# Kernel tuning notes

Measured on AMD Instinct MI355X. Metric: run time of the kernel, lower is better.

The kernel has to match this reference:

```python
import jax, jax.numpy as jnp
import numpy as np

N = 20000      # nodes in both graphs
B = 128        # graphs in batch
E = 320000     # edges (avg degree 16)
F_IN = 768     # num_features (bert/graph feature dim)
RAW_F = 5000   # raw feature dim (hardcoded 5000 in source)
H = 256        # nhid
C = 4          # num_classes


def _gcn(x, src, dst, W, b):
    # PyG GCNConv: add self loops, symmetric D^-1/2 (A+I) D^-1/2 normalization
    n = x.shape[0]
    h = x @ W
    loop = jnp.arange(n, dtype=src.dtype)
    s = jnp.concatenate([src, loop])
    d = jnp.concatenate([dst, loop])
    deg = jax.ops.segment_sum(jnp.ones_like(d, dtype=h.dtype), d, num_segments=n)
    dinv = jax.lax.rsqrt(jnp.maximum(deg, 1.0))
    norm = (dinv[s] * dinv[d])[:, None]
    out = jax.ops.segment_sum(h[s] * norm, d, num_segments=n)
    return out + b


def _segment_mean(x, seg, num_segments):
    s = jax.ops.segment_sum(x, seg, num_segments=num_segments)
    cnt = jax.ops.segment_sum(jnp.ones((x.shape[0],), x.dtype), seg, num_segments=num_segments)
    return s / jnp.maximum(cnt, 1.0)[:, None]


def _prelu(x, a):
    return jnp.where(x >= 0, x, a * x)


def setup_inputs():
    key = jax.random.key(0)
    k = jax.random.split(key, 16)
    graph_x = jax.random.normal(k[0], (N, F_IN), jnp.float32)
    bert_x = jax.random.normal(k[1], (N, F_IN), jnp.float32)
    data_x = jax.random.normal(k[2], (N, RAW_F), jnp.float32) * 0.05
    edge_index = jax.random.randint(k[3], (2, E), 0, N, jnp.int32)
    raw_edge_index = jax.random.randint(k[4], (2, E), 0, N, jnp.int32)
    batch = ((jnp.arange(N) * B) // N).astype(jnp.int32)  # sorted, covers all B graphs
    rootindex = jax.random.randint(k[5], (B,), 0, N, jnp.int32)

    def lin(kk, fin, fout):
        return jax.random.normal(kk, (fin, fout), jnp.float32) * (1.0 / np.sqrt(fin))

    W1 = lin(k[6], F_IN, H); b1 = jnp.zeros((H,), jnp.float32)
    Wc0 = lin(k[7], RAW_F, H); bc0 = jnp.zeros((H,), jnp.float32)
    Wc1 = lin(k[8], H, H); bc1 = jnp.zeros((H,), jnp.float32)
    Wc2 = lin(k[9], H, H); bc2 = jnp.zeros((H,), jnp.float32)
    Wl1 = lin(k[10], 2 * RAW_F, 2 * H); bl1 = jnp.zeros((2 * H,), jnp.float32)
    Wl2 = lin(k[11], 2 * H, H); bl2 = jnp.zeros((H,), jnp.float32)
    W5 = lin(k[12], 5 * H, C); b5 = jnp.zeros((C,), jnp.float32)
    prelu_a = jnp.asarray(0.25, jnp.float32)
    return dict(graph_x=graph_x, bert_x=bert_x, data_x=data_x,
                edge_index=edge_index, raw_edge_index=raw_edge_index,
                graph_batch=batch, x_batch=batch, rootindex=rootindex,
                W1=W1, b1=b1, Wc0=Wc0, bc0=bc0, Wc1=Wc1, bc1=bc1, Wc2=Wc2, bc2=bc2,
                Wl1=Wl1, bl1=bl1, Wl2=Wl2, bl2=bl2, prelu_a=prelu_a, W5=W5, b5=b5)


def reference(graph_x, bert_x, data_x, edge_index, raw_edge_index, graph_batch,
              x_batch, rootindex, W1, b1, Wc0, bc0, Wc1, bc1, Wc2, bc2,
              Wl1, bl1, Wl2, bl2, prelu_a, W5, b5):
    # branch 1: GCNConv over graph_x (bert_user=0), relu, global max pool
    x = jax.nn.relu(_gcn(graph_x, edge_index[0], edge_index[1], W1, b1))
    x = jax.ops.segment_max(x, graph_batch, num_segments=B)   # [B, H]
    # branch 2: scatter_mean of raw features + root node, MLP w/ PReLU (eval: dropout = id)
    new_x = _segment_mean(data_x, x_batch, B)                 # [B, RAW_F]
    root = data_x[rootindex]                                  # [B, RAW_F]
    new_x = jnp.concatenate([new_x, root], axis=1)            # [B, 2*RAW_F]
    new_x = _prelu(new_x @ Wl1 + bl1, prelu_a)
    new_x = _prelu(new_x @ Wl2 + bl2, prelu_a)                # [B, H]
    # branch 3 (boost=1): 3 GCN layers over raw graph, mean pool each layer
    x_one = data_x
    pools = []
    for (W, b) in ((Wc0, bc0), (Wc1, bc1), (Wc2, bc2)):
        x_one = jax.nn.relu(_gcn(x_one, raw_edge_index[0], raw_edge_index[1], W, b))
        pools.append(_segment_mean(x_one, x_batch, B))
    out = jnp.concatenate(pools + [new_x, x], axis=1)         # [B, 5*H]
    return jax.nn.log_softmax(out @ W5 + b5, axis=1)
```

## Files before the change

### kernel.cpp

```cpp
#include <hip/hip_runtime.h>
#include <math.h>

#define NN   20000
#define BG   128
#define EE   320000
#define FIN  768
#define RAWF 5000
#define KP   5120
#define CATK 10240
#define HD   256
#define NC   4

typedef __attribute__((ext_vector_type(4))) float          f32x4;
typedef __attribute__((ext_vector_type(8))) unsigned short u16x8;
typedef __attribute__((ext_vector_type(4))) unsigned short u16x4;
typedef __attribute__((ext_vector_type(8))) __bf16         bf16x8;

__device__ __forceinline__ unsigned short f2bf(float f) {
  unsigned u = __float_as_uint(f);
  u += 0x7FFFu + ((u >> 16) & 1u);
  return (unsigned short)(u >> 16);
}
__device__ __forceinline__ float bf2f(unsigned short u) {
  return __uint_as_float((unsigned)u << 16);
}

static inline int ceil_div(int a, int b) { return (a + b - 1) / b; }

__global__ void count_deg2_k(const int* __restrict__ ei, const int* __restrict__ rei,
                             int* __restrict__ deg1, int* __restrict__ deg2) {
  int i = blockIdx.x * 256 + threadIdx.x;
  if (i < EE) atomicAdd(&deg1[ei[EE + i]], 1);
  else if (i < 2 * EE) atomicAdd(&deg2[rei[i]], 1);
}

__global__ __launch_bounds__(1024) void scan_local_k(const int* __restrict__ deg1,
                                                     const int* __restrict__ deg2,
                                                     int* __restrict__ excl,
                                                     int* __restrict__ bsum, int nb) {
  const int* deg = blockIdx.y ? deg2 : deg1;
  int* ex = excl + (size_t)blockIdx.y * NN;
  int* bs = bsum + (size_t)blockIdx.y * nb;
  __shared__ int wsum[16];
  int t = threadIdx.x, lane = t & 63, w = t >> 6;
  int i = blockIdx.x * 1024 + t;
  int v = (i < NN) ? deg[i] : 0;
  int acc = v;
#pragma unroll
  for (int off = 1; off < 64; off <<= 1) {
    int o = __shfl_up(acc, off, 64);
    if (lane >= off) acc += o;
  }
  if (lane == 63) wsum[w] = acc;
  __syncthreads();
  if (w == 0 && lane < 16) {
    int s = wsum[lane];
#pragma unroll
    for (int off = 1; off < 16; off <<= 1) {
      int o = __shfl_up(s, off, 64);
      if (lane >= off) s += o;
    }
    wsum[lane] = s;
  }
  __syncthreads();
  if (w > 0) acc += wsum[w - 1];
  if (i < NN) ex[i] = acc - v;
  if (t == 1023) bs[blockIdx.x] = acc;
}

__global__ void scan_tops_k(const int* __restrict__ bsum, int* __restrict__ boff,
                            int* __restrict__ end1, int* __restrict__ end2, int nb) {
  int t = threadIdx.x;
  int half = t >> 5, idx = t & 31;
  int v = (idx < nb) ? bsum[half * nb + idx] : 0;
  int acc = v;
#pragma unroll
  for (int off = 1; off < 32; off <<= 1) {
    int o = __shfl_up(acc, off, 32);
    if (idx >= off) acc += o;
  }
  if (idx < nb) boff[half * nb + idx] = acc - v;
  if (idx == nb - 1) {
    if (half == 0) *end1 = acc; else *end2 = acc;
  }
}

__global__ __launch_bounds__(1024) void scan_add_k(
    const int* __restrict__ excl, const int* __restrict__ boff,
    const int* __restrict__ deg1, const int* __restrict__ deg2,
    int* __restrict__ rp1, int* __restrict__ rp2,
    int* __restrict__ cur1, int* __restrict__ cur2,
    float* __restrict__ dv1, float* __restrict__ dv2,
    const int* __restrict__ batch, int* __restrict__ segs, int* __restrict__ sege,
    int nb) {
  int y = blockIdx.y;
  const int* deg = y ? deg2 : deg1;
  int* rp = y ? rp2 : rp1;
  int* cur = y ? cur2 : cur1;
  float* dv = y ? dv2 : dv1;
  int i = blockIdx.x * 1024 + threadIdx.x;
  if (i < NN) {
    int v = excl[(size_t)y * NN + i] + boff[y * nb + blockIdx.x];
    rp[i] = v;
    cur[i] = v;
    dv[i] = rsqrtf((float)(deg[i] + 1));
    if (y == 0) {
      int b = batch[i];
      if (i == 0 || batch[i - 1] != b) segs[b] = i;
      if (i == NN - 1 || batch[i + 1] != b) sege[b] = i + 1;
    }
  }
}

__global__ void scatter_k(const int* __restrict__ ei, const int* __restrict__ rei,
                          int* __restrict__ cur1, int* __restrict__ cur2,
                          int* __restrict__ col1, int* __restrict__ col2) {
  int i = blockIdx.x * 256 + threadIdx.x;
  int y = blockIdx.y;
  if (i < EE) {
    const int* e = y ? rei : ei;
    int* cur = y ? cur2 : cur1;
    int* col = y ? col2 : col1;
    int d = e[EE + i];
    int p = atomicAdd(&cur[d], 1);
    col[p] = e[i];
  }
}

__global__ __launch_bounds__(256) void trans_k(
    const float* __restrict__ i0, unsigned short* __restrict__ o0,
    const float* __restrict__ i1, unsigned short* __restrict__ o1,
    const float* __restrict__ i2, unsigned short* __restrict__ o2,
    const float* __restrict__ i3, unsigned short* __restrict__ o3,
    const float* __restrict__ i4, unsigned short* __restrict__ o4) {
  __shared__ unsigned short tile[32][34];
  int b = blockIdx.x;
  const float* in; unsigned short* out;
  int K, N, Kout, tx, lid;
  if (b < 192)        { in=i0; out=o0; K=768;   N=256; Kout=768;   tx=24;  lid=b; }
  else if (b < 1472)  { in=i1; out=o1; K=5000;  N=256; Kout=5120;  tx=160; lid=b-192; }
  else if (b < 1536)  { in=i2; out=o2; K=256;   N=256; Kout=256;   tx=8;   lid=b-1472; }
  else if (b < 1600)  { in=i3; out=o3; K=256;   N=256; Kout=256;   tx=8;   lid=b-1536; }
  else                { in=i4; out=o4; K=10000; N=512; Kout=10240; tx=320; lid=b-1600; }
  int k0 = (lid % tx) * 32, n0 = (lid / tx) * 32;
  int txx = threadIdx.x & 31, tyy = threadIdx.x >> 5;
#pragma unroll
  for (int r = 0; r < 32; r += 8) {
    int k = k0 + tyy + r, n = n0 + txx;
    float v = (k < K) ? in[(size_t)k * N + n] : 0.f;
    tile[tyy + r][txx] = f2bf(v);
  }
  __syncthreads();
#pragma unroll
  for (int r = 0; r < 32; r += 8) {
    int n = n0 + tyy + r, k = k0 + txx;
    out[(size_t)n * Kout + k] = tile[txx][tyy + r];
  }
}

__global__ __launch_bounds__(256) void conv_pool_k(const float* __restrict__ x,
                                                   unsigned short* __restrict__ xb,
                                                   unsigned short* __restrict__ cat,
                                                   const int* __restrict__ segs,
                                                   const int* __restrict__ sege,
                                                   const int* __restrict__ root) {
  int g = blockIdx.x;
  if (blockIdx.y >= KP / 256) {
    int c = (blockIdx.y - KP / 256) * 256 + threadIdx.x;
    if (c < CATK - RAWF) {
      unsigned short v = 0;
      if (c < RAWF) v = f2bf(x[(size_t)root[g] * RAWF + c]);
      cat[(size_t)g * CATK + RAWF + c] = v;
    }
    return;
  }
  __shared__ f32x4 part[4][64];
  int wave = threadIdx.x >> 6, lane = threadIdx.x & 63;
  int c = blockIdx.y * 256 + lane * 4;
  int s = segs[g], e = sege[g];
  bool v4 = (c + 4 <= RAWF);
  f32x4 sum = (f32x4)0.f;
  for (int i = s + wave; i < e; i += 4) {
    f32x4 v = (f32x4)0.f;
    if (v4) v = *(const f32x4*)(x + (size_t)i * RAWF + c);
    if (xb) {
      u16x4 h;
      h[0] = f2bf(v[0]); h[1] = f2bf(v[1]); h[2] = f2bf(v[2]); h[3] = f2bf(v[3]);
      *(u16x4*)(xb + (size_t)i * KP + c) = h;
    }
    sum += v;
  }
  part[wave][lane] = sum;
  __syncthreads();
  if (threadIdx.x < 64 && v4) {
    f32x4 tot = part[0][lane] + part[1][lane] + part[2][lane] + part[3][lane];
    float cnt = (float)(e - s);
    u16x4 o;
    o[0] = f2bf(tot[0] / cnt); o[1] = f2bf(tot[1] / cnt);
    o[2] = f2bf(tot[2] / cnt); o[3] = f2bf(tot[3] / cnt);
    *(u16x4*)(cat + (size_t)g * CATK + c) = o;
  }
}

template <bool ABF16>
__global__ __launch_bounds__(256) void gemm_k(
    const void* __restrict__ Av, int Astride,
    const unsigned short* __restrict__ Bt, int Bstride,
    float* __restrict__ C, unsigned short* __restrict__ Cb,
    const float* __restrict__ escale,
    int M, int N, int Kreal, int kchunk, int atomic_out) {
  __shared__ unsigned short As[128 * 40];
  __shared__ unsigned short Bs[128 * 40];
  const int tid = threadIdx.x;
  const int lane = tid & 63, wave = tid >> 6;
  const int quad = lane >> 4, l16 = lane & 15;
  const int koff = quad * 8;

  int xt = blockIdx.x, yt = blockIdx.y;
  if (gridDim.x == 2) {
    const int MT = gridDim.y;
    int flat = (yt << 1) | xt;
    int gp = flat >> 4;
    int ybase = gp << 3;
    int rem = MT - ybase;
    int j = flat & 15;
    if (rem >= 8) { xt = j >> 3; yt = ybase + (j & 7); }
    else          { xt = (j >= rem); yt = ybase + (xt ? j - rem : j); }
  }
  const int bn = xt * 128, bm = yt * 128;
  const int wm = (wave >> 1) * 64, wn = (wave & 1) * 64;
  const int kbegin = blockIdx.z * kchunk;
  int kend = kbegin + kchunk; if (kend > Kreal) kend = Kreal;

  const int brow = tid >> 2, bcol = (tid & 3) * 8;
  const int arow_f = tid >> 3, acol_f = (tid & 7) * 4;

  u16x8 pb[2];
  u16x8 pa_b[2];
  f32x4 pa_f[4];

  auto load_tile = [&](int k0) {
#pragma unroll
    for (int i = 0; i < 2; ++i) {
      int gk = k0 + bcol;
      bool ok = ABF16 ? true : (gk + 8 <= kend);
      u16x8 v = (u16x8)(unsigned short)0;
      if (ok) v = *(const u16x8*)(Bt + (size_t)(bn + i * 64 + brow) * Bstride + gk);
      pb[i] = v;
    }
    if (ABF16) {
      const unsigned short* A = (const unsigned short*)Av;
#pragma unroll
      for (int i = 0; i < 2; ++i) {
        int r = bm + i * 64 + brow;
        u16x8 v = (u16x8)(unsigned short)0;
        if (r < M) v = *(const u16x8*)(A + (size_t)r * Astride + k0 + bcol);
        pa_b[i] = v;
      }
    } else {
      const float* A = (const float*)Av;
#pragma unroll
      for (int i = 0; i < 4; ++i) {
        int r = bm + i * 32 + arow_f;
        int gk = k0 + acol_f;
        f32x4 v = (f32x4)0.f;
        if (r < M && gk + 4 <= kend) v = *(const f32x4*)(A + (size_t)r * Astride + gk);
        pa_f[i] = v;
      }
    }
  };
  auto store_tile = [&]() {
#pragma unroll
    for (int i = 0; i < 2; ++i)
      *(u16x8*)&Bs[(i * 64 + brow) * 40 + bcol] = pb[i];
    if (ABF16) {
#pragma unroll
      for (int i = 0; i < 2; ++i)
        *(u16x8*)&As[(i * 64 + brow) * 40 + bcol] = pa_b[i];
    } else {
#pragma unroll
      for (int i = 0; i < 4; ++i) {
        u16x4 h;
        h[0] = f2bf(pa_f[i][0]); h[1] = f2bf(pa_f[i][1]);
        h[2] = f2bf(pa_f[i][2]); h[3] = f2bf(pa_f[i][3]);
        *(u16x4*)&As[(i * 32 + arow_f) * 40 + acol_f] = h;
      }
    }
  };

  f32x4 acc[4][4] = {};
  load_tile(kbegin);
  for (int k0 = kbegin; k0 < kend; k0 += 32) {
    store_tile();
    __syncthreads();
    int k1 = k0 + 32;
    if (k1 < kend) load_tile(k1);
    u16x8 ar[4], br[4];
#pragma unroll
    for (int i = 0; i < 4; ++i) ar[i] = *(const u16x8*)&As[(wm + i * 16 + l16) * 40 + koff];
#pragma unroll
    for (int j = 0; j < 4; ++j) br[j] = *(const u16x8*)&Bs[(wn + j * 16 + l16) * 40 + koff];
#pragma unroll
    for (int i = 0; i < 4; ++i)
#pragma unroll
      for (int j = 0; j < 4; ++j)
        acc[i][j] = __builtin_amdgcn_mfma_f32_16x16x32_bf16(
            __builtin_bit_cast(bf16x8, ar[i]), __builtin_bit_cast(bf16x8, br[j]),
            acc[i][j], 0, 0, 0);
    __syncthreads();
  }
#pragma unroll
  for (int i = 0; i < 4; ++i)
#pragma unroll
    for (int rr = 0; rr < 4; ++rr) {
      int grow = bm + wm + i * 16 + quad * 4 + rr;
      if (grow >= M) continue;
      float sc = escale ? escale[grow] : 1.f;
#pragma unroll
      for (int j = 0; j < 4; ++j) {
        int gcol = bn + wn + j * 16 + l16;
        if (gcol >= N) continue;
        float v = acc[i][j][rr] * sc;
        if (Cb) Cb[(size_t)grow * N + gcol] = f2bf(v);
        else if (atomic_out) atomicAdd(&C[(size_t)grow * N + gcol], v);
        else C[(size_t)grow * N + gcol] = v;
      }
    }
}

__global__ void conv_h_k(const float* __restrict__ in, unsigned short* __restrict__ out) {
  size_t i = (size_t)(blockIdx.x * 256 + threadIdx.x) * 8;
  f32x4 a = *(const f32x4*)(in + i);
  f32x4 b = *(const f32x4*)(in + i + 4);
  u16x8 o;
  o[0]=f2bf(a[0]); o[1]=f2bf(a[1]); o[2]=f2bf(a[2]); o[3]=f2bf(a[3]);
  o[4]=f2bf(b[0]); o[5]=f2bf(b[1]); o[6]=f2bf(b[2]); o[7]=f2bf(b[3]);
  *(u16x8*)(out + i) = o;
}

__global__ __launch_bounds__(256) void gcn_agg_k(
    const unsigned short* __restrict__ hb, const int* __restrict__ rowptr,
    const int* __restrict__ col, const float* __restrict__ dinv,
    const float* __restrict__ bias, unsigned short* __restrict__ outb, int n) {
  int wave = threadIdx.x >> 6, lane = threadIdx.x & 63;
  int node = blockIdx.x * 4 + wave;
  if (node >= n) return;
  int f = lane * 4;
  u16x4 sv = *(const u16x4*)(hb + (size_t)node * HD + f);
  f32x4 acc;
  acc[0] = bf2f(sv[0]); acc[1] = bf2f(sv[1]); acc[2] = bf2f(sv[2]); acc[3] = bf2f(sv[3]);
  int beg = rowptr[node], end = rowptr[node + 1];
  int e = beg;
  for (; e + 4 <= end; e += 4) {
    int s0 = col[e], s1 = col[e + 1], s2 = col[e + 2], s3 = col[e + 3];
    u16x4 h0 = *(const u16x4*)(hb + (size_t)s0 * HD + f);
    u16x4 h1 = *(const u16x4*)(hb + (size_t)s1 * HD + f);
    u16x4 h2 = *(const u16x4*)(hb + (size_t)s2 * HD + f);
    u16x4 h3 = *(const u16x4*)(hb + (size_t)s3 * HD + f);
#pragma unroll
    for (int q = 0; q < 4; ++q)
      acc[q] += bf2f(h0[q]) + bf2f(h1[q]) + bf2f(h2[q]) + bf2f(h3[q]);
  }
  for (; e < end; ++e) {
    u16x4 h0 = *(const u16x4*)(hb + (size_t)col[e] * HD + f);
#pragma unroll
    for (int q = 0; q < 4; ++q) acc[q] += bf2f(h0[q]);
  }
  float di = dinv[node];
  f32x4 b = *(const f32x4*)(bias + f);
  acc = acc * di + b;
  u16x4 o;
#pragma unroll
  for (int q = 0; q < 4; ++q) o[q] = f2bf(fmaxf(acc[q], 0.f));
  *(u16x4*)(outb + (size_t)node * HD + f) = o;
}

__global__ __launch_bounds__(256) void seg_pool_bf16_k(const unsigned short* __restrict__ src,
                                                       const int* __restrict__ segs,
                                                       const int* __restrict__ sege,
                                                       float* __restrict__ dst, int dstride,
                                                       int doff, int mode) {
  int g = blockIdx.x, f = threadIdx.x;
  int s = segs[g], e = sege[g];
  float a0, a1, a2, a3;
  if (mode == 1) { a0 = a1 = a2 = a3 = -INFINITY; } else { a0 = a1 = a2 = a3 = 0.f; }
  int i = s;
  for (; i + 4 <= e; i += 4) {
    float v0 = bf2f(src[(size_t)(i + 0) * HD + f]);
    float v1 = bf2f(src[(size_t)(i + 1) * HD + f]);
    float v2 = bf2f(src[(size_t)(i + 2) * HD + f]);
    float v3 = bf2f(src[(size_t)(i + 3) * HD + f]);
    if (mode == 1) { a0 = fmaxf(a0, v0); a1 = fmaxf(a1, v1); a2 = fmaxf(a2, v2); a3 = fmaxf(a3, v3); }
    else           { a0 += v0; a1 += v1; a2 += v2; a3 += v3; }
  }
  for (; i < e; ++i) {
    float v = bf2f(src[(size_t)i * HD + f]);
    if (mode == 1) a0 = fmaxf(a0, v); else a0 += v;
  }
  float acc;
  if (mode == 1) acc = fmaxf(fmaxf(a0, a1), fmaxf(a2, a3));
  else {
    acc = (a0 + a1) + (a2 + a3);
    acc /= (float)((e - s) > 0 ? (e - s) : 1);
  }
  dst[(size_t)g * dstride + doff + f] = acc;
}

__global__ __launch_bounds__(256) void gemm_e_k(const float* __restrict__ Cd,
                                                const float* __restrict__ bl1,
                                                const float* __restrict__ Wl2,
                                                const float* __restrict__ bl2,
                                                const float* __restrict__ pa,
                                                float* __restrict__ pools) {
  __shared__ float t[512];
  int b = blockIdx.x, n = threadIdx.x;
  float a = *pa;
  for (int k = n; k < 512; k += 256) {
    float v = Cd[(size_t)b * 512 + k] + bl1[k];
    t[k] = (v >= 0.f) ? v : a * v;
  }
  __syncthreads();
  float acc = 0.f;
  for (int k = 0; k < 512; ++k) acc = fmaf(t[k], Wl2[k * 256 + n], acc);
  acc += bl2[n];
  acc = (acc >= 0.f) ? acc : a * acc;
  pools[(size_t)b * 1280 + 768 + n] = acc;
}

__global__ __launch_bounds__(256) void final_k(const float* __restrict__ pools,
                                               const float* __restrict__ W5,
                                               const float* __restrict__ b5,
                                               float* __restrict__ out) {
  __shared__ float red[256][4];
  int b = blockIdx.x, t = threadIdx.x;
  float a0 = 0, a1 = 0, a2 = 0, a3 = 0;
  for (int i = t; i < 1280; i += 256) {
    float p = pools[(size_t)b * 1280 + i];
    a0 = fmaf(p, W5[i * 4 + 0], a0);
    a1 = fmaf(p, W5[i * 4 + 1], a1);
    a2 = fmaf(p, W5[i * 4 + 2], a2);
    a3 = fmaf(p, W5[i * 4 + 3], a3);
  }
  red[t][0] = a0; red[t][1] = a1; red[t][2] = a2; red[t][3] = a3;
  __syncthreads();
  for (int off = 128; off >= 1; off >>= 1) {
    if (t < off)
      for (int c = 0; c < 4; ++c) red[t][c] += red[t + off][c];
    __syncthreads();
  }
  if (t == 0) {
    float z[4];
    for (int c = 0; c < 4; ++c) z[c] = red[0][c] + b5[c];
    float m = fmaxf(fmaxf(z[0], z[1]), fmaxf(z[2], z[3]));
    float s = 0.f;
    for (int c = 0; c < 4; ++c) s += expf(z[c] - m);
    float lse = logf(s);
    for (int c = 0; c < 4; ++c) out[b * 4 + c] = z[c] - m - lse;
  }
}

extern "C" void kernel_launch(void* const* d_in, const int* in_sizes, int n_in,
                              void* d_out, int out_size, void* d_ws, size_t ws_size,
                              hipStream_t stream) {
  const float* graph_x = (const float*)d_in[0];
  const float* data_x  = (const float*)d_in[2];
  const int*   ei      = (const int*)d_in[3];
  const int*   rei     = (const int*)d_in[4];
  const int*   batch   = (const int*)d_in[5];
  const int*   rooti   = (const int*)d_in[7];
  const float* W1  = (const float*)d_in[8];   const float* b1  = (const float*)d_in[9];
  const float* Wc0 = (const float*)d_in[10];  const float* bc0 = (const float*)d_in[11];
  const float* Wc1 = (const float*)d_in[12];  const float* bc1 = (const float*)d_in[13];
  const float* Wc2 = (const float*)d_in[14];  const float* bc2 = (const float*)d_in[15];
  const float* Wl1 = (const float*)d_in[16];  const float* bl1 = (const float*)d_in[17];
  const float* Wl2 = (const float*)d_in[18];  const float* bl2 = (const float*)d_in[19];
  const float* pa  = (const float*)d_in[20];
  const float* W5  = (const float*)d_in[21];  const float* b5  = (const float*)d_in[22];
  float* out = (float*)d_out;

  char* ws = (char*)d_ws;
  size_t off = 0;
  auto take = [&](size_t bytes) -> void* {
    void* p = ws + off;
    off += (bytes + 255) & ~(size_t)255;
    return p;
  };
  const int NB = ceil_div(NN, 1024);

  int *deg1, *deg2, *rp1, *rp2, *cur1, *cur2, *col1, *col2, *excl, *bsum, *boff, *segs, *sege;
  float *dv1, *dv2, *hA, *Cd, *pools;
  unsigned short *W1t, *Wc0t, *Wc1t, *Wc2t, *Wl1t, *catb, *hAb, *hBb, *Axb;

  auto alloc_all = [&](bool withAxb) {
    off = 0;
    deg1 = (int*)take(NN * 4);   deg2 = (int*)take(NN * 4);
    Cd   = (float*)take((size_t)BG * 512 * 4);
    rp1  = (int*)take((NN + 1) * 4); rp2 = (int*)take((NN + 1) * 4);
    cur1 = (int*)take(NN * 4);   cur2 = (int*)take(NN * 4);
    col1 = (int*)take(EE * 4);   col2 = (int*)take(EE * 4);
    dv1  = (float*)take(NN * 4); dv2  = (float*)take(NN * 4);
    excl = (int*)take((size_t)2 * NN * 4);
    bsum = (int*)take(2 * NB * 4); boff = (int*)take(2 * NB * 4);
    segs = (int*)take(BG * 4);   sege = (int*)take(BG * 4);
    W1t  = (unsigned short*)take((size_t)HD * FIN * 2);
    Wc0t = (unsigned short*)take((size_t)HD * KP * 2);
    Wc1t = (unsigned short*)take((size_t)HD * HD * 2);
    Wc2t = (unsigned short*)take((size_t)HD * HD * 2);
    Wl1t = (unsigned short*)take((size_t)512 * CATK * 2);
    catb = (unsigned short*)take((size_t)BG * CATK * 2);
    Axb  = withAxb ? (unsigned short*)take((size_t)NN * KP * 2) : nullptr;
    hA   = (float*)take((size_t)NN * HD * 4);
    hAb  = (unsigned short*)take((size_t)NN * HD * 2);
    hBb  = (unsigned short*)take((size_t)NN * HD * 2);
    pools = (float*)take((size_t)BG * 1280 * 4);
  };
  alloc_all(true);
  if (off > ws_size) alloc_all(false);
  const bool pathA = (Axb != nullptr);

  const size_t degpad = ((size_t)NN * 4 + 255) & ~(size_t)255;
  hipMemsetAsync(deg1, 0, degpad * 2 + (size_t)BG * 512 * 4, stream);

  count_deg2_k<<<ceil_div(2 * EE, 256), 256, 0, stream>>>(ei, rei, deg1, deg2);
  scan_local_k<<<dim3(NB, 2), 1024, 0, stream>>>(deg1, deg2, excl, bsum, NB);
  scan_tops_k<<<1, 64, 0, stream>>>(bsum, boff, rp1 + NN, rp2 + NN, NB);
  scan_add_k<<<dim3(NB, 2), 1024, 0, stream>>>(excl, boff, deg1, deg2, rp1, rp2,
                                               cur1, cur2, dv1, dv2,
                                               batch, segs, sege, NB);
  scatter_k<<<dim3(ceil_div(EE, 256), 2), 256, 0, stream>>>(ei, rei, cur1, cur2, col1, col2);

  trans_k<<<6720, 256, 0, stream>>>(W1, W1t, Wc0, Wc0t, Wc1, Wc1t, Wc2, Wc2t, Wl1, Wl1t);

  conv_pool_k<<<dim3(BG, KP / 256 + ceil_div(CATK - RAWF, 256)), 256, 0, stream>>>(
      data_x, Axb, catb, segs, sege, rooti);

  int mt = ceil_div(NN, 128);

  gemm_k<false><<<dim3(2, mt, 1), 256, 0, stream>>>(graph_x, FIN, W1t, FIN,
                                                    nullptr, hAb, dv1,
                                                    NN, HD, FIN, FIN, 0);
  gcn_agg_k<<<ceil_div(NN, 4), 256, 0, stream>>>(hAb, rp1, col1, dv1, b1, hBb, NN);
  seg_pool_bf16_k<<<BG, 256, 0, stream>>>(hBb, segs, sege, pools, 1280, 1024, 1);

  hipMemsetAsync(hA, 0, (size_t)NN * HD * 4, stream);
  if (pathA)
    gemm_k<true><<<dim3(2, mt, 2), 256, 0, stream>>>(Axb, KP, Wc0t, KP, hA, nullptr, dv2,
                                                     NN, HD, KP, 2560, 1);
  else
    gemm_k<false><<<dim3(2, mt, 4), 256, 0, stream>>>(data_x, RAWF, Wc0t, KP, hA, nullptr, dv2,
                                                      NN, HD, RAWF, 1280, 1);
  conv_h_k<<<(NN * HD) / (256 * 8), 256, 0, stream>>>(hA, hAb);
  gcn_agg_k<<<ceil_div(NN, 4), 256, 0, stream>>>(hAb, rp2, col2, dv2, bc0, hBb, NN);
  seg_pool_bf16_k<<<BG, 256, 0, stream>>>(hBb, segs, sege, pools, 1280, 0, 0);

  gemm_k<true><<<dim3(2, mt, 1), 256, 0, stream>>>(hBb, HD, Wc1t, HD,
                                                   nullptr, hAb, dv2,
                                                   NN, HD, HD, HD, 0);
  gcn_agg_k<<<ceil_div(NN, 4), 256, 0, stream>>>(hAb, rp2, col2, dv2, bc1, hBb, NN);
  seg_pool_bf16_k<<<BG, 256, 0, stream>>>(hBb, segs, sege, pools, 1280, 256, 0);

  gemm_k<true><<<dim3(2, mt, 1), 256, 0, stream>>>(hBb, HD, Wc2t, HD,
                                                   nullptr, hAb, dv2,
                                                   NN, HD, HD, HD, 0);
  gcn_agg_k<<<ceil_div(NN, 4), 256, 0, stream>>>(hAb, rp2, col2, dv2, bc2, hBb, NN);
  seg_pool_bf16_k<<<BG, 256, 0, stream>>>(hBb, segs, sege, pools, 1280, 512, 0);

  gemm_k<true><<<dim3(4, 1, 32), 256, 0, stream>>>(catb, CATK, Wl1t, CATK, Cd, nullptr, nullptr,
                                                   BG, 512, CATK, 320, 1);
  gemm_e_k<<<BG, 256, 0, stream>>>(Cd, bl1, Wl2, bl2, pa, pools);

  final_k<<<BG, 256, 0, stream>>>(pools, W5, b5, out);
}
```

Measured before the change: 1.198 ms.

## Fuse graph pipeline kernels: single-block scan, merged prep kernel, aggregate-with-pool

Replaces the three-kernel CSR scan with one 1024-thread block and merges edge scatter, weight transposes and the feature mean-pool into a single launch. Segment pooling now happens inside the GCN aggregation through shared and global atomics, and the mean divide is deferred to the final kernel. The first-layer GEMM drops split-K and writes bf16 directly, which removes the fp32 buffer, its memset and the conversion kernel. Risks: the single-block scan is serial, the GEMM has less parallelism without split-K, global atomics contend, and the max-pool atomicMax on float bits depends on values being non-negative after ReLU.

```diff
diff --git a/kernel.cpp b/kernel.cpp
--- a/kernel.cpp
+++ b/kernel.cpp
@@ -34,139 +34,118 @@
   else if (i < 2 * EE) atomicAdd(&deg2[rei[i]], 1);
 }
 
-__global__ __launch_bounds__(1024) void scan_local_k(const int* __restrict__ deg1,
-                                                     const int* __restrict__ deg2,
-                                                     int* __restrict__ excl,
-                                                     int* __restrict__ bsum, int nb) {
-  const int* deg = blockIdx.y ? deg2 : deg1;
-  int* ex = excl + (size_t)blockIdx.y * NN;
-  int* bs = bsum + (size_t)blockIdx.y * nb;
-  __shared__ int wsum[16];
-  int t = threadIdx.x, lane = t & 63, w = t >> 6;
-  int i = blockIdx.x * 1024 + t;
-  int v = (i < NN) ? deg[i] : 0;
-  int acc = v;
-#pragma unroll
-  for (int off = 1; off < 64; off <<= 1) {
-    int o = __shfl_up(acc, off, 64);
-    if (lane >= off) acc += o;
-  }
-  if (lane == 63) wsum[w] = acc;
-  __syncthreads();
-  if (w == 0 && lane < 16) {
-    int s = wsum[lane];
-#pragma unroll
-    for (int off = 1; off < 16; off <<= 1) {
-      int o = __shfl_up(s, off, 64);
-      if (lane >= off) s += o;
-    }
-    wsum[lane] = s;
-  }
-  __syncthreads();
-  if (w > 0) acc += wsum[w - 1];
-  if (i < NN) ex[i] = acc - v;
-  if (t == 1023) bs[blockIdx.x] = acc;
-}
-
-__global__ void scan_tops_k(const int* __restrict__ bsum, int* __restrict__ boff,
-                            int* __restrict__ end1, int* __restrict__ end2, int nb) {
-  int t = threadIdx.x;
-  int half = t >> 5, idx = t & 31;
-  int v = (idx < nb) ? bsum[half * nb + idx] : 0;
-  int acc = v;
-#pragma unroll
-  for (int off = 1; off < 32; off <<= 1) {
-    int o = __shfl_up(acc, off, 32);
-    if (idx >= off) acc += o;
-  }
-  if (idx < nb) boff[half * nb + idx] = acc - v;
-  if (idx == nb - 1) {
-    if (half == 0) *end1 = acc; else *end2 = acc;
-  }
-}
-
-__global__ __launch_bounds__(1024) void scan_add_k(
-    const int* __restrict__ excl, const int* __restrict__ boff,
+__global__ __launch_bounds__(1024) void csr_scan_k(
     const int* __restrict__ deg1, const int* __restrict__ deg2,
     int* __restrict__ rp1, int* __restrict__ rp2,
     int* __restrict__ cur1, int* __restrict__ cur2,
     float* __restrict__ dv1, float* __restrict__ dv2,
-    const int* __restrict__ batch, int* __restrict__ segs, int* __restrict__ sege,
-    int nb) {
-  int y = blockIdx.y;
-  const int* deg = y ? deg2 : deg1;
-  int* rp = y ? rp2 : rp1;
-  int* cur = y ? cur2 : cur1;
-  float* dv = y ? dv2 : dv1;
-  int i = blockIdx.x * 1024 + threadIdx.x;
-  if (i < NN) {
-    int v = excl[(size_t)y * NN + i] + boff[y * nb + blockIdx.x];
-    rp[i] = v;
-    cur[i] = v;
-    dv[i] = rsqrtf((float)(deg[i] + 1));
-    if (y == 0) {
-      int b = batch[i];
-      if (i == 0 || batch[i - 1] != b) segs[b] = i;
-      if (i == NN - 1 || batch[i + 1] != b) sege[b] = i + 1;
-    }
-  }
-}
-
-__global__ void scatter_k(const int* __restrict__ ei, const int* __restrict__ rei,
-                          int* __restrict__ cur1, int* __restrict__ cur2,
-                          int* __restrict__ col1, int* __restrict__ col2) {
-  int i = blockIdx.x * 256 + threadIdx.x;
-  int y = blockIdx.y;
-  if (i < EE) {
-    const int* e = y ? rei : ei;
-    int* cur = y ? cur2 : cur1;
-    int* col = y ? col2 : col1;
-    int d = e[EE + i];
-    int p = atomicAdd(&cur[d], 1);
-    col[p] = e[i];
-  }
-}
-
-__global__ __launch_bounds__(256) void trans_k(
+    const int* __restrict__ batch, int* __restrict__ segs, int* __restrict__ sege) {
+  __shared__ int wsum[16];
+  int t = threadIdx.x, lane = t & 63, w = t >> 6;
+  int b0 = t * 20; if (b0 > NN) b0 = NN;
+  int b1 = b0 + 20; if (b1 > NN) b1 = NN;
+#pragma unroll
+  for (int g = 0; g < 2; ++g) {
+    const int* deg = g ? deg2 : deg1;
+    int* rp  = g ? rp2 : rp1;
+    int* cur = g ? cur2 : cur1;
+    float* dv = g ? dv2 : dv1;
+    int sum = 0;
+    for (int i = b0; i < b1; ++i) sum += deg[i];
+    int acc = sum;
+#pragma unroll
+    for (int off = 1; off < 64; off <<= 1) {
+      int o = __shfl_up(acc, off, 64);
+      if (lane >= off) acc += o;
+    }
+    if (lane == 63) wsum[w] = acc;
+    __syncthreads();
+    if (w == 0 && lane < 16) {
+      int s = wsum[lane];
+#pragma unroll
+      for (int off = 1; off < 16; off <<= 1) {
+        int o = __shfl_up(s, off, 64);
+        if (lane >= off) s += o;
+      }
+      wsum[lane] = s;
+    }
+    __syncthreads();
+    int run = (acc - sum) + (w > 0 ? wsum[w - 1] : 0);
+    for (int i = b0; i < b1; ++i) {
+      int v = deg[i];
+      rp[i] = run; cur[i] = run;
+      dv[i] = rsqrtf((float)(v + 1));
+      run += v;
+    }
+    if (t == 0) rp[NN] = wsum[15];
+    __syncthreads();
+  }
+  for (int i = t; i < NN; i += 1024) {
+    int b = batch[i];
+    if (i == 0 || batch[i - 1] != b) segs[b] = i;
+    if (i == NN - 1 || batch[i + 1] != b) sege[b] = i + 1;
+  }
+}
+
+__global__ __launch_bounds__(256) void mid_k(
+    const int* __restrict__ ei, const int* __restrict__ rei,
+    int* __restrict__ cur1, int* __restrict__ cur2,
+    int* __restrict__ col1, int* __restrict__ col2,
     const float* __restrict__ i0, unsigned short* __restrict__ o0,
     const float* __restrict__ i1, unsigned short* __restrict__ o1,
     const float* __restrict__ i2, unsigned short* __restrict__ o2,
     const float* __restrict__ i3, unsigned short* __restrict__ o3,
-    const float* __restrict__ i4, unsigned short* __restrict__ o4) {
+    const float* __restrict__ i4, unsigned short* __restrict__ o4,
+    const float* __restrict__ x, unsigned short* __restrict__ xb,
+    unsigned short* __restrict__ cat,
+    const int* __restrict__ segs, const int* __restrict__ sege,
+    const int* __restrict__ root) {
   __shared__ unsigned short tile[32][34];
-  int b = blockIdx.x;
-  const float* in; unsigned short* out;
-  int K, N, Kout, tx, lid;
-  if (b < 192)        { in=i0; out=o0; K=768;   N=256; Kout=768;   tx=24;  lid=b; }
-  else if (b < 1472)  { in=i1; out=o1; K=5000;  N=256; Kout=5120;  tx=160; lid=b-192; }
-  else if (b < 1536)  { in=i2; out=o2; K=256;   N=256; Kout=256;   tx=8;   lid=b-1472; }
-  else if (b < 1600)  { in=i3; out=o3; K=256;   N=256; Kout=256;   tx=8;   lid=b-1536; }
-  else                { in=i4; out=o4; K=10000; N=512; Kout=10240; tx=320; lid=b-1600; }
-  int k0 = (lid % tx) * 32, n0 = (lid / tx) * 32;
-  int txx = threadIdx.x & 31, tyy = threadIdx.x >> 5;
-#pragma unroll
-  for (int r = 0; r < 32; r += 8) {
-    int k = k0 + tyy + r, n = n0 + txx;
-    float v = (k < K) ? in[(size_t)k * N + n] : 0.f;
-    tile[tyy + r][txx] = f2bf(v);
-  }
-  __syncthreads();
-#pragma unroll
-  for (int r = 0; r < 32; r += 8) {
-    int n = n0 + tyy + r, k = k0 + txx;
-    out[(size_t)n * Kout + k] = tile[txx][tyy + r];
-  }
-}
-
-__global__ __launch_bounds__(256) void conv_pool_k(const float* __restrict__ x,
-                                                   unsigned short* __restrict__ xb,
-                                                   unsigned short* __restrict__ cat,
-                                                   const int* __restrict__ segs,
-                                                   const int* __restrict__ sege,
-                                                   const int* __restrict__ root) {
-  int g = blockIdx.x;
-  if (blockIdx.y >= KP / 256) {
-    int c = (blockIdx.y - KP / 256) * 256 + threadIdx.x;
+  __shared__ f32x4 part[4][64];
+  int b = blockIdx.x, tid = threadIdx.x;
+
+  if (b < 2500) {
+    int y = (b >= 1250);
+    int i = (b - y * 1250) * 256 + tid;
+    if (i < EE) {
+      const int* e = y ? rei : ei;
+      int* cur = y ? cur2 : cur1;
+      int* col = y ? col2 : col1;
+      int d = e[EE + i];
+      int p = atomicAdd(&cur[d], 1);
+      col[p] = e[i];
+    }
+    return;
+  }
+  if (b < 9220) {
+    int bb = b - 2500;
+    const float* in; unsigned short* out;
+    int K, N, Kout, tx, lid;
+    if (bb < 192)        { in=i0; out=o0; K=768;   N=256; Kout=768;   tx=24;  lid=bb; }
+    else if (bb < 1472)  { in=i1; out=o1; K=5000;  N=256; Kout=5120;  tx=160; lid=bb-192; }
+    else if (bb < 1536)  { in=i2; out=o2; K=256;   N=256; Kout=256;   tx=8;   lid=bb-1472; }
+    else if (bb < 1600)  { in=i3; out=o3; K=256;   N=256; Kout=256;   tx=8;   lid=bb-1536; }
+    else                 { in=i4; out=o4; K=10000; N=512; Kout=10240; tx=320; lid=bb-1600; }
+    int k0 = (lid % tx) * 32, n0 = (lid / tx) * 32;
+    int txx = tid & 31, tyy = tid >> 5;
+#pragma unroll
+    for (int r = 0; r < 32; r += 8) {
+      int k = k0 + tyy + r, n = n0 + txx;
+      float v = (k < K) ? in[(size_t)k * N + n] : 0.f;
+      tile[tyy + r][txx] = f2bf(v);
+    }
+    __syncthreads();
+#pragma unroll
+    for (int r = 0; r < 32; r += 8) {
+      int n = n0 + tyy + r, k = k0 + txx;
+      out[(size_t)n * Kout + k] = tile[txx][tyy + r];
+    }
+    return;
+  }
+  int q = b - 9220;
+  int g = q & 127, yy = q >> 7;
+  if (yy >= KP / 256) {
+    int c = (yy - KP / 256) * 256 + tid;
     if (c < CATK - RAWF) {
       unsigned short v = 0;
       if (c < RAWF) v = f2bf(x[(size_t)root[g] * RAWF + c]);
@@ -174,9 +153,8 @@
     }
     return;
   }
-  __shared__ f32x4 part[4][64];
-  int wave = threadIdx.x >> 6, lane = threadIdx.x & 63;
-  int c = blockIdx.y * 256 + lane * 4;
+  int wave = tid >> 6, lane = tid & 63;
+  int c = yy * 256 + lane * 4;
   int s = segs[g], e = sege[g];
   bool v4 = (c + 4 <= RAWF);
   f32x4 sum = (f32x4)0.f;
@@ -192,7 +170,7 @@
   }
   part[wave][lane] = sum;
   __syncthreads();
-  if (threadIdx.x < 64 && v4) {
+  if (tid < 64 && v4) {
     f32x4 tot = part[0][lane] + part[1][lane] + part[2][lane] + part[3][lane];
     float cnt = (float)(e - s);
     u16x4 o;
@@ -328,23 +306,19 @@
     }
 }
 
-__global__ void conv_h_k(const float* __restrict__ in, unsigned short* __restrict__ out) {
-  size_t i = (size_t)(blockIdx.x * 256 + threadIdx.x) * 8;
-  f32x4 a = *(const f32x4*)(in + i);
-  f32x4 b = *(const f32x4*)(in + i + 4);
-  u16x8 o;
-  o[0]=f2bf(a[0]); o[1]=f2bf(a[1]); o[2]=f2bf(a[2]); o[3]=f2bf(a[3]);
-  o[4]=f2bf(b[0]); o[5]=f2bf(b[1]); o[6]=f2bf(b[2]); o[7]=f2bf(b[3]);
-  *(u16x8*)(out + i) = o;
-}
-
-__global__ __launch_bounds__(256) void gcn_agg_k(
+__global__ __launch_bounds__(256) void gcn_agg_pool_k(
     const unsigned short* __restrict__ hb, const int* __restrict__ rowptr,
     const int* __restrict__ col, const float* __restrict__ dinv,
-    const float* __restrict__ bias, unsigned short* __restrict__ outb, int n) {
-  int wave = threadIdx.x >> 6, lane = threadIdx.x & 63;
+    const float* __restrict__ bias, const int* __restrict__ batch,
+    unsigned short* __restrict__ outb, float* __restrict__ pools,
+    int doff, int mode) {
+  __shared__ float red[2][256];
+  int tid = threadIdx.x;
+  int wave = tid >> 6, lane = tid & 63;
   int node = blockIdx.x * 4 + wave;
-  if (node >= n) return;
+  red[0][tid] = 0.f;
+  red[1][tid] = 0.f;
+  __syncthreads();
   int f = lane * 4;
   u16x4 sv = *(const u16x4*)(hb + (size_t)node * HD + f);
   f32x4 acc;
@@ -368,42 +342,32 @@
   }
   float di = dinv[node];
   f32x4 b = *(const f32x4*)(bias + f);
-  acc = acc * di + b;
-  u16x4 o;
-#pragma unroll
-  for (int q = 0; q < 4; ++q) o[q] = f2bf(fmaxf(acc[q], 0.f));
-  *(u16x4*)(outb + (size_t)node * HD + f) = o;
-}
-
-__global__ __launch_bounds__(256) void seg_pool_bf16_k(const unsigned short* __restrict__ src,
-                                                       const int* __restrict__ segs,
-                                                       const int* __restrict__ sege,
-                                                       float* __restrict__ dst, int dstride,
-                                                       int doff, int mode) {
-  int g = blockIdx.x, f = threadIdx.x;
-  int s = segs[g], e = sege[g];
-  float a0, a1, a2, a3;
-  if (mode == 1) { a0 = a1 = a2 = a3 = -INFINITY; } else { a0 = a1 = a2 = a3 = 0.f; }
-  int i = s;
-  for (; i + 4 <= e; i += 4) {
-    float v0 = bf2f(src[(size_t)(i + 0) * HD + f]);
-    float v1 = bf2f(src[(size_t)(i + 1) * HD + f]);
-    float v2 = bf2f(src[(size_t)(i + 2) * HD + f]);
-    float v3 = bf2f(src[(size_t)(i + 3) * HD + f]);
-    if (mode == 1) { a0 = fmaxf(a0, v0); a1 = fmaxf(a1, v1); a2 = fmaxf(a2, v2); a3 = fmaxf(a3, v3); }
-    else           { a0 += v0; a1 += v1; a2 += v2; a3 += v3; }
-  }
-  for (; i < e; ++i) {
-    float v = bf2f(src[(size_t)i * HD + f]);
-    if (mode == 1) a0 = fmaxf(a0, v); else a0 += v;
-  }
-  float acc;
-  if (mode == 1) acc = fmaxf(fmaxf(a0, a1), fmaxf(a2, a3));
-  else {
-    acc = (a0 + a1) + (a2 + a3);
-    acc /= (float)((e - s) > 0 ? (e - s) : 1);
-  }
-  dst[(size_t)g * dstride + doff + f] = acc;
+#pragma unroll
+  for (int q = 0; q < 4; ++q) acc[q] = fmaxf(acc[q] * di + b[q], 0.f);
+  int g0 = batch[blockIdx.x * 4];
+  int slot = batch[node] - g0;
+  if (mode == 0) {
+#pragma unroll
+    for (int q = 0; q < 4; ++q) atomicAdd(&red[slot][f + q], acc[q]);
+  } else {
+#pragma unroll
+    for (int q = 0; q < 4; ++q)
+      atomicMax((unsigned*)&red[slot][f + q], __float_as_uint(acc[q]));
+  }
+  if (outb) {
+    u16x4 o;
+#pragma unroll
+    for (int q = 0; q < 4; ++q) o[q] = f2bf(acc[q]);
+    *(u16x4*)(outb + (size_t)node * HD + f) = o;
+  }
+  __syncthreads();
+  int nslot = batch[blockIdx.x * 4 + 3] - g0 + 1;
+  for (int s = 0; s < nslot; ++s) {
+    float v = red[s][tid];
+    float* dst = &pools[(size_t)(g0 + s) * 1280 + doff + tid];
+    if (mode == 0) atomicAdd(dst, v);
+    else atomicMax((unsigned*)dst, __float_as_uint(v));
+  }
 }
 
 __global__ __launch_bounds__(256) void gemm_e_k(const float* __restrict__ Cd,
@@ -430,12 +394,16 @@
 __global__ __launch_bounds__(256) void final_k(const float* __restrict__ pools,
                                                const float* __restrict__ W5,
                                                const float* __restrict__ b5,
+                                               const int* __restrict__ segs,
+                                               const int* __restrict__ sege,
                                                float* __restrict__ out) {
   __shared__ float red[256][4];
   int b = blockIdx.x, t = threadIdx.x;
+  float rcnt = 1.f / (float)(sege[b] - segs[b]);
   float a0 = 0, a1 = 0, a2 = 0, a3 = 0;
   for (int i = t; i < 1280; i += 256) {
     float p = pools[(size_t)b * 1280 + i];
+    if (i < 768) p *= rcnt;
     a0 = fmaf(p, W5[i * 4 + 0], a0);
     a1 = fmaf(p, W5[i * 4 + 1], a1);
     a2 = fmaf(p, W5[i * 4 + 2], a2);
@@ -485,22 +453,20 @@
     off += (bytes + 255) & ~(size_t)255;
     return p;
   };
-  const int NB = ceil_div(NN, 1024);
-
-  int *deg1, *deg2, *rp1, *rp2, *cur1, *cur2, *col1, *col2, *excl, *bsum, *boff, *segs, *sege;
-  float *dv1, *dv2, *hA, *Cd, *pools;
+
+  int *deg1, *deg2, *rp1, *rp2, *cur1, *cur2, *col1, *col2, *segs, *sege;
+  float *dv1, *dv2, *Cd, *pools;
   unsigned short *W1t, *Wc0t, *Wc1t, *Wc2t, *Wl1t, *catb, *hAb, *hBb, *Axb;
 
   auto alloc_all = [&](bool withAxb) {
     off = 0;
     deg1 = (int*)take(NN * 4);   deg2 = (int*)take(NN * 4);
     Cd   = (float*)take((size_t)BG * 512 * 4);
+    pools = (float*)take((size_t)BG * 1280 * 4);
     rp1  = (int*)take((NN + 1) * 4); rp2 = (int*)take((NN + 1) * 4);
     cur1 = (int*)take(NN * 4);   cur2 = (int*)take(NN * 4);
     col1 = (int*)take(EE * 4);   col2 = (int*)take(EE * 4);
     dv1  = (float*)take(NN * 4); dv2  = (float*)take(NN * 4);
-    excl = (int*)take((size_t)2 * NN * 4);
-    bsum = (int*)take(2 * NB * 4); boff = (int*)take(2 * NB * 4);
     segs = (int*)take(BG * 4);   sege = (int*)take(BG * 4);
     W1t  = (unsigned short*)take((size_t)HD * FIN * 2);
     Wc0t = (unsigned short*)take((size_t)HD * KP * 2);
@@ -509,65 +475,60 @@
     Wl1t = (unsigned short*)take((size_t)512 * CATK * 2);
     catb = (unsigned short*)take((size_t)BG * CATK * 2);
     Axb  = withAxb ? (unsigned short*)take((size_t)NN * KP * 2) : nullptr;
-    hA   = (float*)take((size_t)NN * HD * 4);
     hAb  = (unsigned short*)take((size_t)NN * HD * 2);
     hBb  = (unsigned short*)take((size_t)NN * HD * 2);
-    pools = (float*)take((size_t)BG * 1280 * 4);
   };
   alloc_all(true);
   if (off > ws_size) alloc_all(false);
   const bool pathA = (Axb != nullptr);
 
   const size_t degpad = ((size_t)NN * 4 + 255) & ~(size_t)255;
-  hipMemsetAsync(deg1, 0, degpad * 2 + (size_t)BG * 512 * 4, stream);
+  hipMemsetAsync(deg1, 0,
+                 degpad * 2 + (size_t)BG * 512 * 4 + (size_t)BG * 1280 * 4, stream);
 
   count_deg2_k<<<ceil_div(2 * EE, 256), 256, 0, stream>>>(ei, rei, deg1, deg2);
-  scan_local_k<<<dim3(NB, 2), 1024, 0, stream>>>(deg1, deg2, excl, bsum, NB);
-  scan_tops_k<<<1, 64, 0, stream>>>(bsum, boff, rp1 + NN, rp2 + NN, NB);
-  scan_add_k<<<dim3(NB, 2), 1024, 0, stream>>>(excl, boff, deg1, deg2, rp1, rp2,
-                                               cur1, cur2, dv1, dv2,
-                                               batch, segs, sege, NB);
-  scatter_k<<<dim3(ceil_div(EE, 256), 2), 256, 0, stream>>>(ei, rei, cur1, cur2, col1, col2);
-
-  trans_k<<<6720, 256, 0, stream>>>(W1, W1t, Wc0, Wc0t, Wc1, Wc1t, Wc2, Wc2t, Wl1, Wl1t);
-
-  conv_pool_k<<<dim3(BG, KP / 256 + ceil_div(CATK - RAWF, 256)), 256, 0, stream>>>(
+  csr_scan_k<<<1, 1024, 0, stream>>>(deg1, deg2, rp1, rp2, cur1, cur2,
+                                     dv1, dv2, batch, segs, sege);
+  mid_k<<<2500 + 6720 + 5248, 256, 0, stream>>>(
+      ei, rei, cur1, cur2, col1, col2,
+      W1, W1t, Wc0, Wc0t, Wc1, Wc1t, Wc2, Wc2t, Wl1, Wl1t,
       data_x, Axb, catb, segs, sege, rooti);
 
-  int mt = ceil_div(NN, 128);
+  const int mt = ceil_div(NN, 128);
 
   gemm_k<false><<<dim3(2, mt, 1), 256, 0, stream>>>(graph_x, FIN, W1t, FIN,
                                                     nullptr, hAb, dv1,
                                                     NN, HD, FIN, FIN, 0);
-  gcn_agg_k<<<ceil_div(NN, 4), 256, 0, stream>>>(hAb, rp1, col1, dv1, b1, hBb, NN);
-  seg_pool_bf16_k<<<BG, 256, 0, stream>>>(hBb, segs, sege, pools, 1280, 1024, 1);
-
-  hipMemsetAsync(hA, 0, (size_t)NN * HD * 4, stream);
+  gcn_agg_pool_k<<<NN / 4, 256, 0, stream>>>(hAb, rp1, col1, dv1, b1, batch,
+                                             nullptr, pools, 1024, 1);
+
   if (pathA)
-    gemm_k<true><<<dim3(2, mt, 2), 256, 0, stream>>>(Axb, KP, Wc0t, KP, hA, nullptr, dv2,
-                                                     NN, HD, KP, 2560, 1);
+    gemm_k<true><<<dim3(2, mt, 1), 256, 0, stream>>>(Axb, KP, Wc0t, KP,
+                                                     nullptr, hAb, dv2,
+                                                     NN, HD, KP, KP, 0);
   else
-    gemm_k<false><<<dim3(2, mt, 4), 256, 0, stream>>>(data_x, RAWF, Wc0t, KP, hA, nullptr, dv2,
-                                                      NN, HD, RAWF, 1280, 1);
-  conv_h_k<<<(NN * HD) / (256 * 8), 256, 0, stream>>>(hA, hAb);
-  gcn_agg_k<<<ceil_div(NN, 4), 256, 0, stream>>>(hAb, rp2, col2, dv2, bc0, hBb, NN);
-  seg_pool_bf16_k<<<BG, 256, 0, stream>>>(hBb, segs, sege, pools, 1280, 0, 0);
+    gemm_k<false><<<dim3(2, mt, 1), 256, 0, stream>>>(data_x, RAWF, Wc0t, KP,
+                                                      nullptr, hAb, dv2,
+                                                      NN, HD, RAWF, RAWF, 0);
+  gcn_agg_pool_k<<<NN / 4, 256, 0, stream>>>(hAb, rp2, col2, dv2, bc0, batch,
+                                             hBb, pools, 0, 0);
 
   gemm_k<true><<<dim3(2, mt, 1), 256, 0, stream>>>(hBb, HD, Wc1t, HD,
                                                    nullptr, hAb, dv2,
                                                    NN, HD, HD, HD, 0);
-  gcn_agg_k<<<ceil_div(NN, 4), 256, 0, stream>>>(hAb, rp2, col2, dv2, bc1, hBb, NN);
-  seg_pool_bf16_k<<<BG, 256, 0, stream>>>(hBb, segs, sege, pools, 1280, 256, 0);
+  gcn_agg_pool_k<<<NN / 4, 256, 0, stream>>>(hAb, rp2, col2, dv2, bc1, batch,
+                                             hBb, pools, 256, 0);
 
   gemm_k<true><<<dim3(2, mt, 1), 256, 0, stream>>>(hBb, HD, Wc2t, HD,
                                                    nullptr, hAb, dv2,
                                                    NN, HD, HD, HD, 0);
-  gcn_agg_k<<<ceil_div(NN, 4), 256, 0, stream>>>(hAb, rp2, col2, dv2, bc2, hBb, NN);
-  seg_pool_bf16_k<<<BG, 256, 0, stream>>>(hBb, segs, sege, pools, 1280, 512, 0);
-
-  gemm_k<true><<<dim3(4, 1, 32), 256, 0, stream>>>(catb, CATK, Wl1t, CATK, Cd, nullptr, nullptr,
+  gcn_agg_pool_k<<<NN / 4, 256, 0, stream>>>(hAb, rp2, col2, dv2, bc2, batch,
+                                             nullptr, pools, 512, 0);
+
+  gemm_k<true><<<dim3(4, 1, 32), 256, 0, stream>>>(catb, CATK, Wl1t, CATK,
+                                                   Cd, nullptr, nullptr,
                                                    BG, 512, CATK, 320, 1);
   gemm_e_k<<<BG, 256, 0, stream>>>(Cd, bl1, Wl2, bl2, pa, pools);
 
-  final_k<<<BG, 256, 0, stream>>>(pools, W5, b5, out);
-}
+  final_k<<<BG, 256, 0, stream>>>(pools, W5, b5, segs, sege, out);
+}
```

Result: slower. 1.287 ms (+7.5%).
